# Kernel optimization log

Hardware: AMD Instinct MI355X
Metric: run time of the kernel (lower is better)

## Reference

```python
import jax, jax.numpy as jnp
import numpy as np

N = 50000      # nodes
E = 800000     # edges
H = 4          # heads
C = 64         # hidden per head
HC = H * C     # 256
IN = 2         # in_channels
ED = 1         # edge_dim
NREST = 2      # num_layers - 1


def setup_inputs() -> dict:
    key = jax.random.key(0)
    ks = jax.random.split(key, 32)
    w = lambda i, shape: jax.random.normal(ks[i], shape, jnp.float32) * 0.1
    return {
        "x": jax.random.normal(ks[0], (N, IN), jnp.float32),
        "edge_index": jax.random.randint(ks[1], (2, E), 0, N),
        "edge_attr": jax.random.normal(ks[2], (E, ED), jnp.float32),
        # layer 0 (in_channels=2 -> 256)
        "l0_Wq": w(3, (IN, HC)), "l0_bq": w(4, (HC,)),
        "l0_Wk": w(5, (IN, HC)), "l0_bk": w(6, (HC,)),
        "l0_Wv": w(7, (IN, HC)), "l0_bv": w(8, (HC,)),
        "l0_We": w(9, (ED, HC)),
        "l0_Wskip": w(10, (IN, HC)), "l0_bskip": w(11, (HC,)),
        # layers 1..2 stacked (256 -> 256)
        "r_Wq": w(12, (NREST, HC, HC)), "r_bq": w(13, (NREST, HC)),
        "r_Wk": w(14, (NREST, HC, HC)), "r_bk": w(15, (NREST, HC)),
        "r_Wv": w(16, (NREST, HC, HC)), "r_bv": w(17, (NREST, HC)),
        "r_We": w(18, (NREST, ED, HC)),
        "r_Wskip": w(19, (NREST, HC, HC)), "r_bskip": w(20, (NREST, HC)),
        # classifier
        "cls_W1": w(21, (HC, 128)), "cls_b1": w(22, (128,)),
        "cls_W2": w(23, (128, 1)), "cls_b2": w(24, (1,)),
    }


def transformer_conv(x, src, dst, edge_attr, Wq, bq, Wk, bk, Wv, bv, We, Wskip, bskip):
    # x: [N, Din]; src/dst: [E]; edge_attr: [E, ED]
    n = x.shape[0]
    q = (x @ Wq + bq).reshape(n, H, C)[dst]            # [E,H,C] query at target
    k = (x @ Wk + bk).reshape(n, H, C)[src]            # [E,H,C]
    v = (x @ Wv + bv).reshape(n, H, C)[src]            # [E,H,C]
    e = (edge_attr @ We).reshape(-1, H, C)             # [E,H,C]
    k = k + e
    alpha = (q * k).sum(-1) / jnp.sqrt(jnp.float32(C))  # [E,H]
    # segment softmax over incoming edges of each dst node
    m = jax.ops.segment_max(alpha, dst, num_segments=n)   # [N,H]
    a = jnp.exp(alpha - m[dst])
    s = jax.ops.segment_sum(a, dst, num_segments=n)       # [N,H]
    a = a / (s[dst] + 1e-16)
    msg = a[..., None] * (v + e)                           # [E,H,C]
    out = jax.ops.segment_sum(msg, dst, num_segments=n).reshape(n, HC)
    return out + x @ Wskip + bskip                         # root skip connection


def reference(x, edge_index, edge_attr,
              l0_Wq, l0_bq, l0_Wk, l0_bk, l0_Wv, l0_bv, l0_We, l0_Wskip, l0_bskip,
              r_Wq, r_bq, r_Wk, r_bk, r_Wv, r_bv, r_We, r_Wskip, r_bskip,
              cls_W1, cls_b1, cls_W2, cls_b2):
    src, dst = edge_index[0], edge_index[1]
    h = transformer_conv(x, src, dst, edge_attr,
                         l0_Wq, l0_bq, l0_Wk, l0_bk, l0_Wv, l0_bv,
                         l0_We, l0_Wskip, l0_bskip)
    h = jax.nn.relu(h)  # dropout is a no-op in eval mode
    for i in range(NREST):
        h = transformer_conv(h, src, dst, edge_attr,
                             r_Wq[i], r_bq[i], r_Wk[i], r_bk[i], r_Wv[i], r_bv[i],
                             r_We[i], r_Wskip[i], r_bskip[i])
        h = jax.nn.relu(h)
    out = jax.nn.relu(h @ cls_W1 + cls_b1) @ cls_W2 + cls_b2  # [N,1]
    return out
```

## Files before the change

### kernel.cpp

```cpp
#include <hip/hip_runtime.h>
#include <cstddef>

#define NN 50000
#define NE 800000
#define HCH 256
#define MPAD 50048

typedef __attribute__((ext_vector_type(4))) float f32x4;
typedef __attribute__((ext_vector_type(8))) short s16x8;
typedef __attribute__((ext_vector_type(8))) unsigned short u16x8;
typedef unsigned int uint32;

__device__ inline float bf2f(unsigned short u) {
    return __uint_as_float(((unsigned int)u) << 16);
}
__device__ inline unsigned short f2bf(float f) {
    unsigned int x = __float_as_uint(f);
    x += 0x7FFFu + ((x >> 16) & 1u);
    return (unsigned short)(x >> 16);
}

__global__ void k_hist(const int* __restrict__ dst, int* __restrict__ deg, int e) {
    int i = blockIdx.x * blockDim.x + threadIdx.x;
    if (i < e) atomicAdd(&deg[dst[i]], 1);
}

__global__ __launch_bounds__(1024) void k_scan_a(const int* __restrict__ deg,
                                                 int* __restrict__ incl,
                                                 int* __restrict__ btot, int n) {
    __shared__ int buf[1024];
    int t = threadIdx.x;
    int i = blockIdx.x * 1024 + t;
    int v = (i < n) ? deg[i] : 0;
    buf[t] = v;
    __syncthreads();
    #pragma unroll
    for (int s = 1; s < 1024; s <<= 1) {
        int tv = (t >= s) ? buf[t - s] : 0;
        __syncthreads();
        buf[t] += tv;
        __syncthreads();
    }
    if (i < n) incl[i] = buf[t];
    if (t == 1023) btot[blockIdx.x] = buf[1023];
}

__global__ __launch_bounds__(1024) void k_scan_c(const int* __restrict__ deg,
                                                 const int* __restrict__ incl,
                                                 const int* __restrict__ btot,
                                                 int* __restrict__ off,
                                                 int* __restrict__ cur, int n, int nb) {
    __shared__ int bsh;
    int t = threadIdx.x;
    if (t < 64) {
        int v = (t < nb && t < (int)blockIdx.x) ? btot[t] : 0;
        #pragma unroll
        for (int m = 1; m < 64; m <<= 1) v += __shfl_xor(v, m);
        if (t == 0) bsh = v;
    }
    __syncthreads();
    int bbase = bsh;
    int i = blockIdx.x * 1024 + t;
    if (i < n) {
        int inc = bbase + incl[i];
        off[i + 1] = inc;
        cur[i] = inc - deg[i];
    }
    if (i == 0) off[0] = 0;
}

__global__ void k_scatter(const int* __restrict__ src, const int* __restrict__ dst,
                          const float* __restrict__ attr, int* __restrict__ cur,
                          int2* __restrict__ csr, int e) {
    int i = blockIdx.x * blockDim.x + threadIdx.x;
    if (i < e) {
        int d = dst[i];
        int pos = atomicAdd(&cur[d], 1);
        csr[pos] = make_int2(src[i], __float_as_int(attr[i]));
    }
}

struct PackSrc { const float* w[9]; };
__global__ void k_prep(PackSrc ps, unsigned short* __restrict__ Bt,
                       unsigned short* __restrict__ W1t, int* __restrict__ deg,
                       const float* __restrict__ Wq, const float* __restrict__ bq,
                       const float* __restrict__ Wk, const float* __restrict__ bk,
                       const float* __restrict__ We, float* __restrict__ gram) {
    int b = blockIdx.x;
    if (b < 2176) {
        int i = b * 256 + threadIdx.x;
        if (i < 524288) {
            int mi = i >> 16;
            int elem = i & 65535;
            int n = elem >> 8, k = elem & 255;
            Bt[i] = f2bf(ps.w[mi][(size_t)k * 256 + n]);
        } else {
            int e = i - 524288;
            int n = e >> 8, k = e & 255;
            W1t[e] = f2bf(ps.w[8][(size_t)k * 128 + n]);
        }
    } else if (b < 2176 + 196) {
        int i = (b - 2176) * 256 + threadIdx.x;
        if (i < NN) deg[i] = 0;
    } else {
        int t = threadIdx.x;
        if (t < 48) {
            int h = t / 12, q = t % 12, i = q >> 2, j = q & 3;
            const float* a = (i < 2) ? Wq + i * HCH + h * 64 : bq + h * 64;
            const float* bb = (j == 0) ? Wk + h * 64
                            : (j == 1) ? Wk + HCH + h * 64
                            : (j == 2) ? bk + h * 64
                                       : We + h * 64;
            float s = 0.f;
            for (int c = 0; c < 64; ++c) s = fmaf(a[c], bb[c], s);
            gram[h * 16 + i * 4 + j] = s;
        }
    }
}

__global__ __launch_bounds__(256) void k_agg0(
    const float* __restrict__ x, const int* __restrict__ off,
    const int2* __restrict__ csr, const float* __restrict__ gram,
    const float* __restrict__ Wv, const float* __restrict__ bv,
    const float* __restrict__ We, const float* __restrict__ Wsk,
    const float* __restrict__ bsk,
    unsigned short* __restrict__ Ho, int nnodes) {
    int n = blockIdx.x * 8 + (threadIdx.x >> 5);
    if (n >= nnodes) return;
    int s = threadIdx.x & 31;
    float xd0 = x[n * 2], xd1 = x[n * 2 + 1];

    float t0[4], t1[4], t2[4], ta[4];
    #pragma unroll
    for (int h = 0; h < 4; ++h) {
        const float* g = gram + h * 16;
        t0[h] = (xd0 * g[0] + xd1 * g[4] + g[8])  * 0.125f;
        t1[h] = (xd0 * g[1] + xd1 * g[5] + g[9])  * 0.125f;
        t2[h] = (xd0 * g[2] + xd1 * g[6] + g[10]) * 0.125f;
        ta[h] = (xd0 * g[3] + xd1 * g[7] + g[11]) * 0.125f;
    }

    float S0[4] = {0,0,0,0}, S1[4] = {0,0,0,0}, S2[4] = {0,0,0,0}, SE[4] = {0,0,0,0};
    int e0 = off[n], e1 = off[n + 1];
    for (int e = e0 + s; e < e1; e += 32) {
        int2 ee = csr[e];
        float2 xs = ((const float2*)x)[ee.x];
        float attr = __int_as_float(ee.y);
        #pragma unroll
        for (int h = 0; h < 4; ++h) {
            float alpha = fmaf(t0[h], xs.x, fmaf(t1[h], xs.y, fmaf(ta[h], attr, t2[h])));
            float w = __expf(fminf(alpha, 60.f));
            S0[h] = fmaf(w, xs.x, S0[h]);
            S1[h] = fmaf(w, xs.y, S1[h]);
            S2[h] += w;
            SE[h] = fmaf(w, attr, SE[h]);
        }
    }
    #pragma unroll
    for (int m = 1; m < 32; m <<= 1) {
        #pragma unroll
        for (int h = 0; h < 4; ++h) {
            S0[h] += __shfl_xor(S0[h], m);
            S1[h] += __shfl_xor(S1[h], m);
            S2[h] += __shfl_xor(S2[h], m);
            SE[h] += __shfl_xor(SE[h], m);
        }
    }
    int hs = s >> 3;
    float inv = 1.f / (S2[hs] + 1e-16f);
    float s0 = S0[hs], s1 = S1[hs], s2 = S2[hs], se = SE[hs];
    int cbase = s * 8;
    u16x8 o;
    #pragma unroll
    for (int c = 0; c < 8; ++c) {
        int ch = cbase + c;
        float msg = (s0 * Wv[ch] + s1 * Wv[HCH + ch] + s2 * bv[ch] + se * We[ch]) * inv;
        float val = msg + xd0 * Wsk[ch] + xd1 * Wsk[HCH + ch] + bsk[ch];
        o[c] = f2bf(fmaxf(val, 0.f));
    }
    *(u16x8*)(Ho + (size_t)n * HCH + cbase) = o;
}

struct GOut4 {
    unsigned short* o[4];
    const float* b[4];
};

__global__ __launch_bounds__(256) void k_mfma4(
    const unsigned short* __restrict__ A, const unsigned short* __restrict__ Bt,
    GOut4 g, int M) {
    __shared__ __align__(16) unsigned short As[2][128 * 32];
    __shared__ __align__(16) unsigned short Bs[2][128 * 32];
    const int t = threadIdx.x, wid = t >> 6, l = t & 63;
    const int v = (blockIdx.x & 7) * 391 + (blockIdx.x >> 3);
    const int m0 = (v >> 3) * 128;
    const int n0 = (v & 7) * 128;
    const int wr = wid >> 1, wc = wid & 1;

    f32x4 acc[4][4];
    #pragma unroll
    for (int m = 0; m < 4; ++m)
        #pragma unroll
        for (int n = 0; n < 4; ++n) acc[m][n] = (f32x4)0.f;

    const int off0 = (wid * 2 + 0) * 1024 + l * 16;
    const int off1 = (wid * 2 + 1) * 1024 + l * 16;
    const int ar0 = off0 >> 6, ac0 = off0 & 63;
    const int ar1 = off1 >> 6, ac1 = off1 & 63;
    const char* Abase = (const char*)A;
    const char* Bbase = (const char*)Bt;
    char* AsB = (char*)As;
    char* BsB = (char*)Bs;

    auto STAGE = [&](int buf, int k0) {
        __builtin_amdgcn_global_load_lds(
            (const __attribute__((address_space(1))) uint32*)(Abase + (size_t)(m0 + ar0) * 512 + k0 * 2 + ac0),
            (__attribute__((address_space(3))) uint32*)(AsB + buf * 8192 + (wid * 2 + 0) * 1024), 16, 0, 0);
        __builtin_amdgcn_global_load_lds(
            (const __attribute__((address_space(1))) uint32*)(Abase + (size_t)(m0 + ar1) * 512 + k0 * 2 + ac1),
            (__attribute__((address_space(3))) uint32*)(AsB + buf * 8192 + (wid * 2 + 1) * 1024), 16, 0, 0);
        __builtin_amdgcn_global_load_lds(
            (const __attribute__((address_space(1))) uint32*)(Bbase + (size_t)(n0 + ar0) * 512 + k0 * 2 + ac0),
            (__attribute__((address_space(3))) uint32*)(BsB + buf * 8192 + (wid * 2 + 0) * 1024), 16, 0, 0);
        __builtin_amdgcn_global_load_lds(
            (const __attribute__((address_space(1))) uint32*)(Bbase + (size_t)(n0 + ar1) * 512 + k0 * 2 + ac1),
            (__attribute__((address_space(3))) uint32*)(BsB + buf * 8192 + (wid * 2 + 1) * 1024), 16, 0, 0);
    };

    STAGE(0, 0);
    __syncthreads();
    int cur = 0;
    for (int tt = 0; tt < 8; ++tt) {
        if (tt < 7) STAGE(cur ^ 1, (tt + 1) * 32);
        s16x8 af[4], bfv[4];
        #pragma unroll
        for (int m = 0; m < 4; ++m)
            af[m] = *(const s16x8*)(As[cur] + (size_t)(wr * 64 + m * 16 + (l & 15)) * 32 + (l >> 4) * 8);
        #pragma unroll
        for (int n = 0; n < 4; ++n)
            bfv[n] = *(const s16x8*)(Bs[cur] + (size_t)(wc * 64 + n * 16 + (l & 15)) * 32 + (l >> 4) * 8);
        #pragma unroll
        for (int m = 0; m < 4; ++m)
            #pragma unroll
            for (int n = 0; n < 4; ++n)
                acc[m][n] = __builtin_amdgcn_mfma_f32_16x16x32_bf16(af[m], bfv[n], acc[m][n], 0, 0, 0);
        __syncthreads();
        cur ^= 1;
    }

    const int mat = n0 >> 8;
    const int colBase = (n0 & 255) + wc * 64;
    const float* bias = g.b[mat];
    unsigned short* O = g.o[mat];
    #pragma unroll
    for (int n = 0; n < 4; ++n) {
        int col = colBase + n * 16 + (l & 15);
        float bv = bias[col];
        #pragma unroll
        for (int m = 0; m < 4; ++m) {
            int row0 = m0 + wr * 64 + m * 16 + (l >> 4) * 4;
            #pragma unroll
            for (int r = 0; r < 4; ++r) {
                int row = row0 + r;
                if (row < M)
                    O[(size_t)row * HCH + col] = f2bf(acc[m][n][r] + bv);
            }
        }
    }
}

__global__ __launch_bounds__(256) void k_cls(
    const unsigned short* __restrict__ A, const unsigned short* __restrict__ Bt,
    const float* __restrict__ b1, const float* __restrict__ W2,
    const float* __restrict__ b2, float* __restrict__ out, int M) {
    __shared__ __align__(16) unsigned short As[128 * 32];
    __shared__ __align__(16) unsigned short Bs[128 * 32];
    const int t = threadIdx.x, wid = t >> 6, l = t & 63;
    const int m0 = blockIdx.x * 128;
    const int wr = wid >> 1, wc = wid & 1;

    f32x4 acc[4][4];
    #pragma unroll
    for (int m = 0; m < 4; ++m)
        #pragma unroll
        for (int n = 0; n < 4; ++n) acc[m][n] = (f32x4)0.f;

    const int off0 = (wid * 2 + 0) * 1024 + l * 16;
    const int off1 = (wid * 2 + 1) * 1024 + l * 16;
    const int ar0 = off0 >> 6, ac0 = off0 & 63;
    const int ar1 = off1 >> 6, ac1 = off1 & 63;
    const char* Abase = (const char*)A;
    const char* Bbase = (const char*)Bt;
    char* AsB = (char*)As;
    char* BsB = (char*)Bs;

    for (int k0 = 0; k0 < 256; k0 += 32) {
        __builtin_amdgcn_global_load_lds(
            (const __attribute__((address_space(1))) uint32*)(Abase + (size_t)(m0 + ar0) * 512 + k0 * 2 + ac0),
            (__attribute__((address_space(3))) uint32*)(AsB + (wid * 2 + 0) * 1024), 16, 0, 0);
        __builtin_amdgcn_global_load_lds(
            (const __attribute__((address_space(1))) uint32*)(Abase + (size_t)(m0 + ar1) * 512 + k0 * 2 + ac1),
            (__attribute__((address_space(3))) uint32*)(AsB + (wid * 2 + 1) * 1024), 16, 0, 0);
        __builtin_amdgcn_global_load_lds(
            (const __attribute__((address_space(1))) uint32*)(Bbase + (size_t)(ar0)*512 + k0 * 2 + ac0),
            (__attribute__((address_space(3))) uint32*)(BsB + (wid * 2 + 0) * 1024), 16, 0, 0);
        __builtin_amdgcn_global_load_lds(
            (const __attribute__((address_space(1))) uint32*)(Bbase + (size_t)(ar1)*512 + k0 * 2 + ac1),
            (__attribute__((address_space(3))) uint32*)(BsB + (wid * 2 + 1) * 1024), 16, 0, 0);
        __syncthreads();

        s16x8 af[4], bfv[4];
        #pragma unroll
        for (int m = 0; m < 4; ++m)
            af[m] = *(const s16x8*)(As + (size_t)(wr * 64 + m * 16 + (l & 15)) * 32 + (l >> 4) * 8);
        #pragma unroll
        for (int n = 0; n < 4; ++n)
            bfv[n] = *(const s16x8*)(Bs + (size_t)(wc * 64 + n * 16 + (l & 15)) * 32 + (l >> 4) * 8);
        #pragma unroll
        for (int m = 0; m < 4; ++m)
            #pragma unroll
            for (int n = 0; n < 4; ++n)
                acc[m][n] = __builtin_amdgcn_mfma_f32_16x16x32_bf16(af[m], bfv[n], acc[m][n], 0, 0, 0);
        __syncthreads();
    }

    float w2v[4], bv[4];
    #pragma unroll
    for (int n = 0; n < 4; ++n) {
        int col = wc * 64 + n * 16 + (l & 15);
        w2v[n] = W2[col];
        bv[n] = b1[col];
    }
    float partv[16];
    #pragma unroll
    for (int m = 0; m < 4; ++m)
        #pragma unroll
        for (int r = 0; r < 4; ++r) {
            float pv = 0.f;
            #pragma unroll
            for (int n = 0; n < 4; ++n)
                pv = fmaf(fmaxf(acc[m][n][r] + bv[n], 0.f), w2v[n], pv);
            pv += __shfl_xor(pv, 1); pv += __shfl_xor(pv, 2);
            pv += __shfl_xor(pv, 4); pv += __shfl_xor(pv, 8);
            partv[m * 4 + r] = pv;
        }
    float* cbuf = (float*)As;
    if (wc == 0 && (l & 15) == 0) {
        #pragma unroll
        for (int m = 0; m < 4; ++m)
            #pragma unroll
            for (int r = 0; r < 4; ++r)
                cbuf[wr * 64 + m * 16 + (l >> 4) * 4 + r] = partv[m * 4 + r];
    }
    __syncthreads();
    if (wc == 1 && (l & 15) == 0) {
        float b2v = b2[0];
        #pragma unroll
        for (int m = 0; m < 4; ++m)
            #pragma unroll
            for (int r = 0; r < 4; ++r) {
                int rl = wr * 64 + m * 16 + (l >> 4) * 4 + r;
                int row = m0 + rl;
                if (row < M) out[row] = cbuf[rl] + partv[m * 4 + r] + b2v;
            }
    }
}

__global__ __launch_bounds__(256) void k_agg(
    const unsigned short* __restrict__ Q, const unsigned short* __restrict__ K,
    const unsigned short* __restrict__ V, const unsigned short* __restrict__ S,
    const int* __restrict__ off, const int2* __restrict__ csr,
    const float* __restrict__ We,
    unsigned short* __restrict__ Ho, int nnodes) {
    int n = blockIdx.x * 8 + (threadIdx.x >> 5);
    if (n >= nnodes) return;
    int s = threadIdx.x & 31;
    size_t base = (size_t)n * HCH + s * 8;

    u16x8 qu = *(const u16x8*)(Q + base);
    float qf[8], wef[8];
    #pragma unroll
    for (int c = 0; c < 8; ++c) qf[c] = bf2f(qu[c]) * 0.125f;
    float4 we0 = *(const float4*)(We + s * 8);
    float4 we1 = *(const float4*)(We + s * 8 + 4);
    wef[0] = we0.x; wef[1] = we0.y; wef[2] = we0.z; wef[3] = we0.w;
    wef[4] = we1.x; wef[5] = we1.y; wef[6] = we1.z; wef[7] = we1.w;

    float p = 0.f;
    #pragma unroll
    for (int c = 0; c < 8; ++c) p = fmaf(qf[c], wef[c], p);
    p += __shfl_xor(p, 1); p += __shfl_xor(p, 2); p += __shfl_xor(p, 4);
    float qWe = p;

    float ssum = 0.f, accE = 0.f;
    float acc[8];
    #pragma unroll
    for (int c = 0; c < 8; ++c) acc[c] = 0.f;

    int e0 = off[n], e1 = off[n + 1];
    const int laneoff = s * 8;
    for (int idx = e0; idx < e1; idx += 4) {
        u16x8 ku[4], vu[4];
        float at[4];
        bool ok[4];
        #pragma unroll
        for (int j = 0; j < 4; ++j) {
            bool o = (idx + j) < e1;
            int2 ee = o ? csr[idx + j] : make_int2(0, 0);
            ok[j] = o;
            at[j] = __int_as_float(ee.y);
            size_t sb = ((size_t)ee.x << 8) + laneoff;
            ku[j] = *(const u16x8*)(K + sb);
            vu[j] = *(const u16x8*)(V + sb);
        }
        #pragma unroll
        for (int j = 0; j < 4; ++j) {
            float d = 0.f;
            #pragma unroll
            for (int c = 0; c < 8; ++c) d = fmaf(qf[c], bf2f(ku[j][c]), d);
            d += __shfl_xor(d, 1); d += __shfl_xor(d, 2); d += __shfl_xor(d, 4);
            float alpha = fmaf(at[j], qWe, d);
            float w = ok[j] ? __expf(fminf(alpha, 60.f)) : 0.f;
            ssum += w;
            accE = fmaf(w, at[j], accE);
            #pragma unroll
            for (int c = 0; c < 8; ++c) acc[c] = fmaf(w, bf2f(vu[j][c]), acc[c]);
        }
    }

    u16x8 su = *(const u16x8*)(S + base);
    float inv = 1.f / (ssum + 1e-16f);
    u16x8 o;
    #pragma unroll
    for (int c = 0; c < 8; ++c)
        o[c] = f2bf(fmaxf(fmaf(acc[c] + accE * wef[c], inv, bf2f(su[c])), 0.f));
    *(u16x8*)(Ho + base) = o;
}

extern "C" void kernel_launch(void* const* d_in, const int* in_sizes, int n_in,
                              void* d_out, int out_size, void* d_ws, size_t ws_size,
                              hipStream_t stream) {
    const float* x      = (const float*)d_in[0];
    const int*   ei     = (const int*)d_in[1];
    const float* eattr  = (const float*)d_in[2];
    const float* l0_Wq  = (const float*)d_in[3];
    const float* l0_bq  = (const float*)d_in[4];
    const float* l0_Wk  = (const float*)d_in[5];
    const float* l0_bk  = (const float*)d_in[6];
    const float* l0_Wv  = (const float*)d_in[7];
    const float* l0_bv  = (const float*)d_in[8];
    const float* l0_We  = (const float*)d_in[9];
    const float* l0_Wsk = (const float*)d_in[10];
    const float* l0_bsk = (const float*)d_in[11];
    const float* r_Wq   = (const float*)d_in[12];
    const float* r_bq   = (const float*)d_in[13];
    const float* r_Wk   = (const float*)d_in[14];
    const float* r_bk   = (const float*)d_in[15];
    const float* r_Wv   = (const float*)d_in[16];
    const float* r_bv   = (const float*)d_in[17];
    const float* r_We   = (const float*)d_in[18];
    const float* r_Wsk  = (const float*)d_in[19];
    const float* r_bsk  = (const float*)d_in[20];
    const float* cls_W1 = (const float*)d_in[21];
    const float* cls_b1 = (const float*)d_in[22];
    const float* cls_W2 = (const float*)d_in[23];
    const float* cls_b2 = (const float*)d_in[24];
    float* out = (float*)d_out;

    const int* src = ei;
    const int* dst = ei + NE;

    char* p = (char*)d_ws;
    auto alloc = [&](size_t bytes) {
        char* r = p;
        p += (bytes + 255) & ~(size_t)255;
        return r;
    };
    unsigned short* h  = (unsigned short*)alloc((size_t)MPAD * HCH * 2);
    unsigned short* Qb = (unsigned short*)alloc((size_t)NN * HCH * 2);
    unsigned short* Kb = (unsigned short*)alloc((size_t)NN * HCH * 2);
    unsigned short* Vb = (unsigned short*)alloc((size_t)NN * HCH * 2);
    unsigned short* Sb = (unsigned short*)alloc((size_t)NN * HCH * 2);
    unsigned short* Bt = (unsigned short*)alloc((size_t)2 * 1024 * 256 * 2);
    unsigned short* W1t= (unsigned short*)alloc((size_t)128 * 256 * 2);
    float* gram   = (float*)alloc(4 * 16 * 4);
    int* deg      = (int*)alloc((size_t)NN * 4);
    int* incl     = (int*)alloc((size_t)NN * 4);
    int* off      = (int*)alloc((size_t)(NN + 1) * 4);
    int* cur      = (int*)alloc((size_t)NN * 4);
    int* btot     = (int*)alloc(64 * 4);
    int2* csr     = (int2*)alloc((size_t)NE * 8);

    const int NB = (NN + 1023) / 1024;

    PackSrc ps;
    ps.w[0] = r_Wq;  ps.w[1] = r_Wk;  ps.w[2] = r_Wv;  ps.w[3] = r_Wsk;
    ps.w[4] = r_Wq + (size_t)HCH * HCH;  ps.w[5] = r_Wk + (size_t)HCH * HCH;
    ps.w[6] = r_Wv + (size_t)HCH * HCH;  ps.w[7] = r_Wsk + (size_t)HCH * HCH;
    ps.w[8] = cls_W1;
    k_prep<<<2177 + 196, 256, 0, stream>>>(ps, Bt, W1t, deg,
                                           l0_Wq, l0_bq, l0_Wk, l0_bk, l0_We, gram);

    k_hist<<<(NE + 255) / 256, 256, 0, stream>>>(dst, deg, NE);
    k_scan_a<<<NB, 1024, 0, stream>>>(deg, incl, btot, NN);
    k_scan_c<<<NB, 1024, 0, stream>>>(deg, incl, btot, off, cur, NN, NB);
    k_scatter<<<(NE + 255) / 256, 256, 0, stream>>>(src, dst, eattr, cur, csr, NE);

    k_agg0<<<(NN + 7) / 8, 256, 0, stream>>>(x, off, csr, gram,
                                             l0_Wv, l0_bv, l0_We, l0_Wsk, l0_bsk, h, NN);

    const int mt = (NN + 127) / 128;
    for (int i = 0; i < 2; ++i) {
        const unsigned short* Bi = Bt + (size_t)i * 1024 * 256;
        GOut4 g;
        g.o[0] = Qb; g.b[0] = r_bq + (size_t)i * HCH;
        g.o[1] = Kb; g.b[1] = r_bk + (size_t)i * HCH;
        g.o[2] = Vb; g.b[2] = r_bv + (size_t)i * HCH;
        g.o[3] = Sb; g.b[3] = r_bsk + (size_t)i * HCH;
        k_mfma4<<<mt * 8, 256, 0, stream>>>(h, Bi, g, NN);
        k_agg<<<(NN + 7) / 8, 256, 0, stream>>>(Qb, Kb, Vb, Sb, off, csr,
                                                r_We + (size_t)i * HCH, h, NN);
    }

    k_cls<<<mt, 256, 0, stream>>>(h, W1t, cls_b1, cls_W2, cls_b2, out, NN);
}
```

Measured before the change: 531.3 us.

## Split fused attention aggregation into separate alpha and value-aggregation kernels

The single per-node aggregation kernel, which gathered both K and V rows per edge, becomes two passes. The first computes the per-edge softmax weights, writes them to a new edge-by-head buffer, and stores per-node sums. The second re-reads the CSR and weights and gathers V rows to accumulate the output. The likely aim is to halve the live gather footprint per pass and lower register pressure, at the cost of an extra launch, a second CSR read, and roughly 12.8 MB of extra weight traffic per layer.

```diff
diff --git a/kernel.cpp b/kernel.cpp
--- a/kernel.cpp
+++ b/kernel.cpp
@@ -366,12 +366,12 @@
     }
 }
 
-__global__ __launch_bounds__(256) void k_agg(
+__global__ __launch_bounds__(256) void k_alpha(
     const unsigned short* __restrict__ Q, const unsigned short* __restrict__ K,
-    const unsigned short* __restrict__ V, const unsigned short* __restrict__ S,
     const int* __restrict__ off, const int2* __restrict__ csr,
     const float* __restrict__ We,
-    unsigned short* __restrict__ Ho, int nnodes) {
+    float* __restrict__ wbuf, float* __restrict__ SS, float* __restrict__ AE,
+    int nnodes) {
     int n = blockIdx.x * 8 + (threadIdx.x >> 5);
     if (n >= nnodes) return;
     int s = threadIdx.x & 31;
@@ -393,14 +393,12 @@
     float qWe = p;
 
     float ssum = 0.f, accE = 0.f;
-    float acc[8];
-    #pragma unroll
-    for (int c = 0; c < 8; ++c) acc[c] = 0.f;
-
     int e0 = off[n], e1 = off[n + 1];
     const int laneoff = s * 8;
+    const int h = s >> 3;
+    const bool writer = (s & 7) == 0;
     for (int idx = e0; idx < e1; idx += 4) {
-        u16x8 ku[4], vu[4];
+        u16x8 ku[4];
         float at[4];
         bool ok[4];
         #pragma unroll
@@ -409,9 +407,7 @@
             int2 ee = o ? csr[idx + j] : make_int2(0, 0);
             ok[j] = o;
             at[j] = __int_as_float(ee.y);
-            size_t sb = ((size_t)ee.x << 8) + laneoff;
-            ku[j] = *(const u16x8*)(K + sb);
-            vu[j] = *(const u16x8*)(V + sb);
+            ku[j] = *(const u16x8*)(K + ((size_t)ee.x << 8) + laneoff);
         }
         #pragma unroll
         for (int j = 0; j < 4; ++j) {
@@ -423,13 +419,60 @@
             float w = ok[j] ? __expf(fminf(alpha, 60.f)) : 0.f;
             ssum += w;
             accE = fmaf(w, at[j], accE);
-            #pragma unroll
-            for (int c = 0; c < 8; ++c) acc[c] = fmaf(w, bf2f(vu[j][c]), acc[c]);
-        }
-    }
-
+            if (ok[j] && writer) wbuf[(size_t)(idx + j) * 4 + h] = w;
+        }
+    }
+    if (writer) {
+        SS[n * 4 + h] = ssum;
+        AE[n * 4 + h] = accE;
+    }
+}
+
+__global__ __launch_bounds__(256) void k_aggv(
+    const unsigned short* __restrict__ V, const unsigned short* __restrict__ S,
+    const int* __restrict__ off, const int2* __restrict__ csr,
+    const float* __restrict__ wbuf, const float* __restrict__ SS,
+    const float* __restrict__ AE, const float* __restrict__ We,
+    unsigned short* __restrict__ Ho, int nnodes) {
+    int n = blockIdx.x * 8 + (threadIdx.x >> 5);
+    if (n >= nnodes) return;
+    int s = threadIdx.x & 31;
+    size_t base = (size_t)n * HCH + s * 8;
+    const int laneoff = s * 8;
+    const int h = s >> 3;
+
+    float acc[8];
+    #pragma unroll
+    for (int c = 0; c < 8; ++c) acc[c] = 0.f;
+
+    int e0 = off[n], e1 = off[n + 1];
+    for (int idx = e0; idx < e1; idx += 4) {
+        u16x8 vu[4];
+        float w[4];
+        #pragma unroll
+        for (int j = 0; j < 4; ++j) {
+            bool o = (idx + j) < e1;
+            int2 ee = o ? csr[idx + j] : make_int2(0, 0);
+            w[j] = o ? wbuf[(size_t)(idx + j) * 4 + h] : 0.f;
+            vu[j] = *(const u16x8*)(V + ((size_t)ee.x << 8) + laneoff);
+        }
+        #pragma unroll
+        for (int j = 0; j < 4; ++j) {
+            #pragma unroll
+            for (int c = 0; c < 8; ++c) acc[c] = fmaf(w[j], bf2f(vu[j][c]), acc[c]);
+        }
+    }
+
+    float wef[8];
+    float4 we0 = *(const float4*)(We + s * 8);
+    float4 we1 = *(const float4*)(We + s * 8 + 4);
+    wef[0] = we0.x; wef[1] = we0.y; wef[2] = we0.z; wef[3] = we0.w;
+    wef[4] = we1.x; wef[5] = we1.y; wef[6] = we1.z; wef[7] = we1.w;
+
+    float ssum = SS[n * 4 + h];
+    float accE = AE[n * 4 + h];
+    float inv = 1.f / (ssum + 1e-16f);
     u16x8 su = *(const u16x8*)(S + base);
-    float inv = 1.f / (ssum + 1e-16f);
     u16x8 o;
     #pragma unroll
     for (int c = 0; c < 8; ++c)
@@ -484,6 +527,9 @@
     unsigned short* Bt = (unsigned short*)alloc((size_t)2 * 1024 * 256 * 2);
     unsigned short* W1t= (unsigned short*)alloc((size_t)128 * 256 * 2);
     float* gram   = (float*)alloc(4 * 16 * 4);
+    float* wbuf   = (float*)alloc((size_t)NE * 4 * 4);
+    float* SSb    = (float*)alloc((size_t)NN * 4 * 4);
+    float* AEb    = (float*)alloc((size_t)NN * 4 * 4);
     int* deg      = (int*)alloc((size_t)NN * 4);
     int* incl     = (int*)alloc((size_t)NN * 4);
     int* off      = (int*)alloc((size_t)(NN + 1) * 4);
@@ -510,6 +556,7 @@
                                              l0_Wv, l0_bv, l0_We, l0_Wsk, l0_bsk, h, NN);
 
     const int mt = (NN + 127) / 128;
+    const int at = (NN + 7) / 8;
     for (int i = 0; i < 2; ++i) {
         const unsigned short* Bi = Bt + (size_t)i * 1024 * 256;
         GOut4 g;
@@ -518,8 +565,10 @@
         g.o[2] = Vb; g.b[2] = r_bv + (size_t)i * HCH;
         g.o[3] = Sb; g.b[3] = r_bsk + (size_t)i * HCH;
         k_mfma4<<<mt * 8, 256, 0, stream>>>(h, Bi, g, NN);
-        k_agg<<<(NN + 7) / 8, 256, 0, stream>>>(Qb, Kb, Vb, Sb, off, csr,
-                                                r_We + (size_t)i * HCH, h, NN);
+        k_alpha<<<at, 256, 0, stream>>>(Qb, Kb, off, csr, r_We + (size_t)i * HCH,
+                                        wbuf, SSb, AEb, NN);
+        k_aggv<<<at, 256, 0, stream>>>(Vb, Sb, off, csr, wbuf, SSb, AEb,
+                                       r_We + (size_t)i * HCH, h, NN);
     }
 
     k_cls<<<mt, 256, 0, stream>>>(h, W1t, cls_b1, cls_W2, cls_b2, out, NN);
```

New measurement: 552.1 us. 1.04x slower.
